# Kernel tuning notes

Measured on AMD Instinct MI355X. Metric: run time of the kernel, lower is better.

## Reference

```python
import jax, jax.numpy as jnp
import numpy as np

W_IMG = 512
H_IMG = 512
D_MODEL = 192
N_FREQ = 8
LN_EPS = 1e-5


def _fourier_pe(coords_norm):
    # coords_norm: [B,K,2] in [0,1); returns [B,K,4*N_FREQ]
    freqs = 2.0 ** jnp.arange(N_FREQ, dtype=jnp.float32)  # [F]
    two_pi = 2.0 * jnp.pi
    x = coords_norm[..., 0:1] * freqs * two_pi  # [B,K,F]
    y = coords_norm[..., 1:2] * freqs * two_pi
    return jnp.concatenate([jnp.sin(x), jnp.cos(x), jnp.sin(y), jnp.cos(y)], axis=-1)


def _bilinear_sample(feat, gx, gy):
    # feat: [B,C,H,W]; gx,gy: [B,K] normalized coords in [-1,1], align_corners=True
    B, C, H, W = feat.shape
    ix = (gx + 1.0) * 0.5 * (W - 1)
    iy = (gy + 1.0) * 0.5 * (H - 1)
    ix0 = jnp.floor(ix)
    iy0 = jnp.floor(iy)
    wx = ix - ix0  # [B,K]
    wy = iy - iy0
    x0 = jnp.clip(ix0.astype(jnp.int32), 0, W - 1)
    x1 = jnp.clip(ix0.astype(jnp.int32) + 1, 0, W - 1)
    y0 = jnp.clip(iy0.astype(jnp.int32), 0, H - 1)
    y1 = jnp.clip(iy0.astype(jnp.int32) + 1, 0, H - 1)
    b = jnp.arange(B)[:, None]  # [B,1] broadcast against [B,K]
    g = lambda y, x: feat[b, :, y, x]  # [B,K,C]
    out = (g(y0, x0) * ((1 - wx) * (1 - wy))[..., None]
           + g(y0, x1) * (wx * (1 - wy))[..., None]
           + g(y1, x0) * ((1 - wx) * wy)[..., None]
           + g(y1, x1) * (wx * wy)[..., None])
    return out  # [B,K,C]


def setup_inputs() -> dict:
    key = jax.random.key(0)
    ks = jax.random.split(key, 16)
    B, K = 8, 4096
    # pixel coordinates in [0, W_IMG-1] x [0, H_IMG-1]
    u = jax.random.uniform(ks[0], (B, K, 2), dtype=jnp.float32)
    coords = u * jnp.array([W_IMG - 1, H_IMG - 1], dtype=jnp.float32)
    L1 = jax.random.normal(ks[1], (B, D_MODEL, 128, 128), dtype=jnp.float32)
    L2 = jax.random.normal(ks[2], (B, D_MODEL, 64, 64), dtype=jnp.float32)
    L3 = jax.random.normal(ks[3], (B, D_MODEL, 32, 32), dtype=jnp.float32)
    L4 = jax.random.normal(ks[4], (B, D_MODEL, 16, 16), dtype=jnp.float32)
    d_in = D_MODEL * 4 + 4 * N_FREQ  # 800
    Wseed_w = jax.random.normal(ks[5], (D_MODEL, d_in), dtype=jnp.float32) / np.sqrt(d_in)
    Wseed_b = jnp.zeros((D_MODEL,), dtype=jnp.float32)
    ln_g = jnp.ones((D_MODEL,), dtype=jnp.float32)
    ln_b = jnp.zeros((D_MODEL,), dtype=jnp.float32)
    Wpos_w = jax.random.normal(ks[6], (D_MODEL, 4 * N_FREQ), dtype=jnp.float32) / np.sqrt(4 * N_FREQ)
    Wpos_b = jnp.zeros((D_MODEL,), dtype=jnp.float32)
    return {"coords": coords, "L1": L1, "L2": L2, "L3": L3, "L4": L4,
            "Wseed_w": Wseed_w, "Wseed_b": Wseed_b, "ln_g": ln_g, "ln_b": ln_b,
            "Wpos_w": Wpos_w, "Wpos_b": Wpos_b}


def reference(coords, L1, L2, L3, L4, Wseed_w, Wseed_b, ln_g, ln_b, Wpos_w, Wpos_b):
    B, K, _ = coords.shape
    # normalized grid in [-1,1] (x uses W, y uses H), align_corners=True convention
    gx = 2.0 * coords[..., 0] / (W_IMG - 1) - 1.0  # [B,K]
    gy = 2.0 * coords[..., 1] / (H_IMG - 1) - 1.0
    center_grid = jnp.stack([gx, gy], axis=-1).reshape(B, K, 1, 2)
    coords_norm = coords / jnp.array([W_IMG, H_IMG], dtype=jnp.float32)
    pe_q = _fourier_pe(coords_norm)  # [B,K,32]
    f1 = _bilinear_sample(L1, gx, gy)
    f2 = _bilinear_sample(L2, gx, gy)
    f3 = _bilinear_sample(L3, gx, gy)
    f4 = _bilinear_sample(L4, gx, gy)
    x = jnp.concatenate([f1, f2, f3, f4, pe_q], axis=-1)  # [B,K,800]
    seed = x @ Wseed_w.T + Wseed_b
    mu = jnp.mean(seed, axis=-1, keepdims=True)
    var = jnp.mean((seed - mu) ** 2, axis=-1, keepdims=True)
    seed = (seed - mu) / jnp.sqrt(var + LN_EPS) * ln_g + ln_b
    pos = pe_q @ Wpos_w.T + Wpos_b
    return (seed, pos, center_grid)
```

## Files before the change

kernel.cpp:

```cpp
#include <hip/hip_runtime.h>
#include <hip/hip_bf16.h>
#include <stdint.h>

typedef unsigned short u16;
typedef short s16x8 __attribute__((ext_vector_type(8)));
typedef float f32x4 __attribute__((ext_vector_type(4)));
typedef uint32_t u32x4 __attribute__((ext_vector_type(4)));

__device__ __forceinline__ uint32_t pack_bf16(float lo, float hi) {
  float2 f; f.x = lo; f.y = hi;
  __hip_bfloat162 h = __float22bfloat162_rn(f);
  union { __hip_bfloat162 h; uint32_t u; } c; c.h = h;
  return c.u;
}
__device__ __forceinline__ u16 f2bf(float f) {
  union { float f; uint32_t u; } a; a.f = f;
  uint32_t u = a.u;
  return (u16)((u + 0x7fffu + ((u >> 16) & 1u)) >> 16);
}
__device__ __forceinline__ float bf2f(uint32_t hbits) {
  union { uint32_t u; float f; } a; a.u = hbits << 16;
  return a.f;
}

__global__ __launch_bounds__(256) void prep_all(
    const float* __restrict__ L1, const float* __restrict__ L2,
    const float* __restrict__ L3, const float* __restrict__ L4,
    const float* __restrict__ ws_w, const float* __restrict__ wp_w,
    u16* __restrict__ T1, u16* __restrict__ T2,
    u16* __restrict__ T3, u16* __restrict__ T4,
    u16* __restrict__ dWs, u16* __restrict__ dWp) {
  const int bid = blockIdx.x;
  const int t = threadIdx.x;

  if (bid >= 2720) {
    int t0 = (bid - 2720) * 256 + t;
    for (int i = t0; i < 39936; i += 8192) {
      const float* s; u16* d; int off;
      if (i < 38400) { s = ws_w; d = dWs; off = 4 * i; }
      else           { s = wp_w; d = dWp; off = 4 * (i - 38400); }
      f32x4 v = *(const f32x4*)(s + off);
      uint2 o;
      o.x = pack_bf16(v.x, v.y);
      o.y = pack_bf16(v.z, v.w);
      *(uint2*)(d + off) = o;
    }
    return;
  }

  const float* src; u16* dst; int HW, tiles, rel;
  if (bid < 2048)      { src = L1; dst = T1; HW = 16384; tiles = 256; rel = bid; }
  else if (bid < 2560) { src = L2; dst = T2; HW = 4096;  tiles = 64;  rel = bid - 2048; }
  else if (bid < 2688) { src = L3; dst = T3; HW = 1024;  tiles = 16;  rel = bid - 2560; }
  else                 { src = L4; dst = T4; HW = 256;   tiles = 4;   rel = bid - 2688; }
  const int b = rel / tiles, hw0 = (rel % tiles) * 64;

  __shared__ uint32_t tileD[96 * 65];
  const float* sb = src + (size_t)b * 192 * HW + hw0;
  for (int i = 0; i < 6; ++i) {
    int idx = i * 256 + t;
    int c2 = idx >> 4, hw4 = idx & 15;
    f32x4 a = *(const f32x4*)(sb + (size_t)(2 * c2) * HW + hw4 * 4);
    f32x4 c = *(const f32x4*)(sb + (size_t)(2 * c2 + 1) * HW + hw4 * 4);
    uint32_t* w = &tileD[c2 * 65 + hw4 * 4];
    w[0] = pack_bf16(a.x, c.x);
    w[1] = pack_bf16(a.y, c.y);
    w[2] = pack_bf16(a.z, c.z);
    w[3] = pack_bf16(a.w, c.w);
  }
  __syncthreads();
  uint32_t* d = (uint32_t*)(dst + ((size_t)b * HW + hw0) * 192);
  for (int i = 0; i < 12; ++i) {
    int e = i * 256 + t;
    int hw = e / 48, cp = e - hw * 48;
    uint2 v;
    v.x = tileD[(cp * 2) * 65 + hw];
    v.y = tileD[(cp * 2 + 1) * 65 + hw];
    *(uint2*)(d + hw * 96 + cp * 2) = v;
  }
}

__global__ __launch_bounds__(256, 4) void seed_main(
    const float* __restrict__ coords,
    const u16* __restrict__ T1, const u16* __restrict__ T2,
    const u16* __restrict__ T3, const u16* __restrict__ T4,
    const u16* __restrict__ Wseed, const u16* __restrict__ Wpos,
    const float* __restrict__ seed_b, const float* __restrict__ ln_g,
    const float* __restrict__ ln_b, const float* __restrict__ pos_b,
    float* __restrict__ out_seed, float* __restrict__ out_pos,
    float* __restrict__ out_cg) {

  __shared__ __align__(16) u16 xt[16 * 808];
  __shared__ float mu_s[16], rs_s[16];

  const int t = threadIdx.x;
  const int gp0 = blockIdx.x * 16;
  const int b = gp0 >> 12;

  if (t < 32) {
    int p = t >> 1, xy = t & 1;
    float c = coords[(gp0 + p) * 2 + xy];
    out_cg[(gp0 + p) * 2 + xy] = c * (2.0f / 511.0f) - 1.0f;
  }
  for (int i = 0; i < 2; ++i) {
    int e = i * 256 + t;
    int p = e >> 5, j = e & 31;
    float c = coords[(gp0 + p) * 2 + ((j >> 4) & 1)] * (1.0f / 512.0f);
    float v = c * (float)(1 << (j & 7));
    float a = (v - floorf(v)) * 6.283185307179586f;
    float r = (j & 8) ? __cosf(a) : __sinf(a);
    xt[p * 808 + 768 + j] = f2bf(r);
  }

  {
    const u16* B1 = T1 + (size_t)b * 16384 * 192;
    const u16* B2 = T2 + (size_t)b * 4096 * 192;
    const u16* B3 = T3 + (size_t)b * 1024 * 192;
    const u16* B4 = T4 + (size_t)b * 256 * 192;
    int plv = t >> 2;
    int lv = plv & 3, p = plv >> 2;
    int c4b = t & 3;
    float cx = coords[(gp0 + p) * 2 + 0];
    float cy = coords[(gp0 + p) * 2 + 1];
    float gx = cx * (2.0f / 511.0f) - 1.0f;
    float gy = cy * (2.0f / 511.0f) - 1.0f;
    int Wl = 128 >> lv;
    float ix = (gx + 1.0f) * 0.5f * (float)(Wl - 1);
    float iy = (gy + 1.0f) * 0.5f * (float)(Wl - 1);
    float fx = floorf(ix), fy = floorf(iy);
    float wx = ix - fx, wy = iy - fy;
    int x0 = (int)fx, y0 = (int)fy;
    int x1 = min(max(x0 + 1, 0), Wl - 1), y1 = min(max(y0 + 1, 0), Wl - 1);
    x0 = min(max(x0, 0), Wl - 1); y0 = min(max(y0, 0), Wl - 1);
    const u16* base = (lv == 0) ? B1 : (lv == 1) ? B2 : (lv == 2) ? B3 : B4;
    const u16* b00 = base + (y0 * Wl + x0) * 192;
    const u16* b01 = base + (y0 * Wl + x1) * 192;
    const u16* b10 = base + (y1 * Wl + x0) * 192;
    const u16* b11 = base + (y1 * Wl + x1) * 192;
    float w00 = (1.0f - wx) * (1.0f - wy), w01 = wx * (1.0f - wy);
    float w10 = (1.0f - wx) * wy,          w11 = wx * wy;
    u16* dstp = xt + p * 808 + lv * 192;
#pragma unroll
    for (int i = 0; i < 6; ++i) {
      int cc = (c4b + 4 * i) * 8;
      u32x4 q00 = *(const u32x4*)(b00 + cc);
      u32x4 q01 = *(const u32x4*)(b01 + cc);
      u32x4 q10 = *(const u32x4*)(b10 + cc);
      u32x4 q11 = *(const u32x4*)(b11 + cc);
      u32x4 o;
#pragma unroll
      for (int k = 0; k < 4; ++k) {
        float lo = bf2f(q00[k] & 0xffff) * w00 + bf2f(q01[k] & 0xffff) * w01 +
                   bf2f(q10[k] & 0xffff) * w10 + bf2f(q11[k] & 0xffff) * w11;
        float hi = bf2f(q00[k] >> 16) * w00 + bf2f(q01[k] >> 16) * w01 +
                   bf2f(q10[k] >> 16) * w10 + bf2f(q11[k] >> 16) * w11;
        o[k] = pack_bf16(lo, hi);
      }
      *(u32x4*)(dstp + cc) = o;
    }
  }
  __syncthreads();

  const int lid = t & 63, wv = t >> 6;
  const int quad = lid >> 4, mrow = lid & 15;
  const int nt0 = wv * 3;

  f32x4 accS[3], accP[3];
#pragma unroll
  for (int j = 0; j < 3; ++j) { accS[j] = (f32x4)0.0f; accP[j] = (f32x4)0.0f; }

  const u16* wp0 = Wseed + (size_t)((nt0 + 0) * 16 + mrow) * 800 + quad * 8;
  const u16* wp1 = wp0 + 16 * 800;
  const u16* wp2 = wp1 + 16 * 800;
  const u16* arow = xt + mrow * 808 + quad * 8;

  s16x8 a_last;
#pragma unroll 5
  for (int kc = 0; kc < 25; ++kc) {
    int ko = kc * 32;
    s16x8 a = *(const s16x8*)(arow + ko);
    s16x8 b0 = *(const s16x8*)(wp0 + ko);
    s16x8 b1 = *(const s16x8*)(wp1 + ko);
    s16x8 b2 = *(const s16x8*)(wp2 + ko);
    accS[0] = __builtin_amdgcn_mfma_f32_16x16x32_bf16(a, b0, accS[0], 0, 0, 0);
    accS[1] = __builtin_amdgcn_mfma_f32_16x16x32_bf16(a, b1, accS[1], 0, 0, 0);
    accS[2] = __builtin_amdgcn_mfma_f32_16x16x32_bf16(a, b2, accS[2], 0, 0, 0);
    if (kc == 24) a_last = a;
  }
#pragma unroll
  for (int j = 0; j < 3; ++j) {
    int n = (nt0 + j) * 16 + mrow;
    s16x8 bw = *(const s16x8*)(Wpos + n * 32 + quad * 8);
    accP[j] = __builtin_amdgcn_mfma_f32_16x16x32_bf16(a_last, bw, accP[j], 0, 0, 0);
  }

#pragma unroll
  for (int j = 0; j < 3; ++j) {
    int n = (nt0 + j) * 16 + mrow;
    float pb = pos_b[n];
#pragma unroll
    for (int r = 0; r < 4; ++r)
      out_pos[(size_t)(gp0 + quad * 4 + r) * 192 + n] = accP[j][r] + pb;
  }

  __syncthreads();
  float* preLN = (float*)xt;
#pragma unroll
  for (int j = 0; j < 3; ++j) {
    int n = (nt0 + j) * 16 + mrow;
    float sb = seed_b[n];
#pragma unroll
    for (int r = 0; r < 4; ++r)
      preLN[(quad * 4 + r) * 193 + n] = accS[j][r] + sb;
  }
  __syncthreads();

  {
    int r = t >> 4, g = t & 15;
    float s = 0.0f, sq = 0.0f;
#pragma unroll
    for (int i = 0; i < 12; ++i) {
      float v = preLN[r * 193 + g * 12 + i];
      s += v; sq += v * v;
    }
#pragma unroll
    for (int d = 8; d > 0; d >>= 1) {
      s += __shfl_down(s, d, 16);
      sq += __shfl_down(sq, d, 16);
    }
    if (g == 0) {
      float mu = s * (1.0f / 192.0f);
      float var = sq * (1.0f / 192.0f) - mu * mu;
      mu_s[r] = mu;
      rs_s[r] = 1.0f / sqrtf(var + 1e-5f);
    }
  }
  __syncthreads();

  for (int i = 0; i < 12; ++i) {
    int e = i * 256 + t;
    int r = e / 192, n = e - r * 192;
    float v = (preLN[r * 193 + n] - mu_s[r]) * rs_s[r] * ln_g[n] + ln_b[n];
    out_seed[(size_t)(gp0 + r) * 192 + n] = v;
  }
}

extern "C" void kernel_launch(void* const* d_in, const int* in_sizes, int n_in,
                              void* d_out, int out_size, void* d_ws, size_t ws_size,
                              hipStream_t stream) {
  const float* coords  = (const float*)d_in[0];
  const float* L1      = (const float*)d_in[1];
  const float* L2      = (const float*)d_in[2];
  const float* L3      = (const float*)d_in[3];
  const float* L4      = (const float*)d_in[4];
  const float* Wseed_w = (const float*)d_in[5];
  const float* Wseed_b = (const float*)d_in[6];
  const float* ln_g    = (const float*)d_in[7];
  const float* ln_b    = (const float*)d_in[8];
  const float* Wpos_w  = (const float*)d_in[9];
  const float* Wpos_b  = (const float*)d_in[10];

  u16* T1  = (u16*)d_ws;
  u16* T2  = T1 + (size_t)8 * 16384 * 192;
  u16* T3  = T2 + (size_t)8 * 4096 * 192;
  u16* T4  = T3 + (size_t)8 * 1024 * 192;
  u16* Wsd = T4 + (size_t)8 * 256 * 192;
  u16* Wps = Wsd + 153600;

  prep_all<<<2752, 256, 0, stream>>>(L1, L2, L3, L4, Wseed_w, Wpos_w,
                                     T1, T2, T3, T4, Wsd, Wps);

  float* out_seed = (float*)d_out;
  float* out_pos  = out_seed + (size_t)32768 * 192;
  float* out_cg   = out_pos  + (size_t)32768 * 192;

  seed_main<<<2048, 256, 0, stream>>>(coords, T1, T2, T3, T4, Wsd, Wps,
                                      Wseed_b, ln_g, ln_b, Wpos_b,
                                      out_seed, out_pos, out_cg);
}
```

Baseline: 274.9 us.

## Pre-swizzle weights into MFMA fragment order and software-pipeline gather and GEMM loads

```diff
diff --git a/kernel.cpp b/kernel.cpp
--- a/kernel.cpp
+++ b/kernel.cpp
@@ -21,6 +21,20 @@
 __device__ __forceinline__ float bf2f(uint32_t hbits) {
   union { uint32_t u; float f; } a; a.u = hbits << 16;
   return a.f;
+}
+
+__device__ __forceinline__ u32x4 bilin4(u32x4 q00, u32x4 q01, u32x4 q10, u32x4 q11,
+                                        float w00, float w01, float w10, float w11) {
+  u32x4 o;
+#pragma unroll
+  for (int k = 0; k < 4; ++k) {
+    float lo = bf2f(q00[k] & 0xffff) * w00 + bf2f(q01[k] & 0xffff) * w01 +
+               bf2f(q10[k] & 0xffff) * w10 + bf2f(q11[k] & 0xffff) * w11;
+    float hi = bf2f(q00[k] >> 16) * w00 + bf2f(q01[k] >> 16) * w01 +
+               bf2f(q10[k] >> 16) * w10 + bf2f(q11[k] >> 16) * w11;
+    o[k] = pack_bf16(lo, hi);
+  }
+  return o;
 }
 
 __global__ __launch_bounds__(256) void prep_all(
@@ -36,14 +50,31 @@
   if (bid >= 2720) {
     int t0 = (bid - 2720) * 256 + t;
     for (int i = t0; i < 39936; i += 8192) {
-      const float* s; u16* d; int off;
-      if (i < 38400) { s = ws_w; d = dWs; off = 4 * i; }
-      else           { s = wp_w; d = dWp; off = 4 * (i - 38400); }
-      f32x4 v = *(const f32x4*)(s + off);
-      uint2 o;
-      o.x = pack_bf16(v.x, v.y);
-      o.y = pack_bf16(v.z, v.w);
-      *(uint2*)(d + off) = o;
+      if (i < 38400) {
+        int e4 = 4 * i;
+        int n = e4 / 800;
+        int k = e4 - n * 800;
+        f32x4 v = *(const f32x4*)(ws_w + e4);
+        int nt = n >> 4, mrow = n & 15;
+        int kc = k >> 5, quad = (k >> 3) & 3, e0 = k & 7;
+        int dst = ((nt * 25 + kc) * 64 + (quad * 16 + mrow)) * 8 + e0;
+        uint2 o;
+        o.x = pack_bf16(v.x, v.y);
+        o.y = pack_bf16(v.z, v.w);
+        *(uint2*)(dWs + dst) = o;
+      } else {
+        int j = i - 38400;
+        int e4 = 4 * j;
+        int n = e4 >> 5, k = e4 & 31;
+        f32x4 v = *(const f32x4*)(wp_w + e4);
+        int nt = n >> 4, mrow = n & 15;
+        int quad = k >> 3, e0 = k & 7;
+        int dst = (nt * 64 + (quad * 16 + mrow)) * 8 + e0;
+        uint2 o;
+        o.x = pack_bf16(v.x, v.y);
+        o.y = pack_bf16(v.z, v.w);
+        *(uint2*)(dWp + dst) = o;
+      }
     }
     return;
   }
@@ -80,7 +111,7 @@
   }
 }
 
-__global__ __launch_bounds__(256, 4) void seed_main(
+__global__ __launch_bounds__(256, 6) void seed_main(
     const float* __restrict__ coords,
     const u16* __restrict__ T1, const u16* __restrict__ T2,
     const u16* __restrict__ T3, const u16* __restrict__ T4,
@@ -140,24 +171,24 @@
     float w00 = (1.0f - wx) * (1.0f - wy), w01 = wx * (1.0f - wy);
     float w10 = (1.0f - wx) * wy,          w11 = wx * wy;
     u16* dstp = xt + p * 808 + lv * 192;
-#pragma unroll
-    for (int i = 0; i < 6; ++i) {
-      int cc = (c4b + 4 * i) * 8;
-      u32x4 q00 = *(const u32x4*)(b00 + cc);
-      u32x4 q01 = *(const u32x4*)(b01 + cc);
-      u32x4 q10 = *(const u32x4*)(b10 + cc);
-      u32x4 q11 = *(const u32x4*)(b11 + cc);
-      u32x4 o;
-#pragma unroll
-      for (int k = 0; k < 4; ++k) {
-        float lo = bf2f(q00[k] & 0xffff) * w00 + bf2f(q01[k] & 0xffff) * w01 +
-                   bf2f(q10[k] & 0xffff) * w10 + bf2f(q11[k] & 0xffff) * w11;
-        float hi = bf2f(q00[k] >> 16) * w00 + bf2f(q01[k] >> 16) * w01 +
-                   bf2f(q10[k] >> 16) * w10 + bf2f(q11[k] >> 16) * w11;
-        o[k] = pack_bf16(lo, hi);
-      }
-      *(u32x4*)(dstp + cc) = o;
-    }
+    int cph = (c4b + lv) & 3;
+    int cc = cph * 8;
+    u32x4 q00 = *(const u32x4*)(b00 + cc);
+    u32x4 q01 = *(const u32x4*)(b01 + cc);
+    u32x4 q10 = *(const u32x4*)(b10 + cc);
+    u32x4 q11 = *(const u32x4*)(b11 + cc);
+#pragma unroll
+    for (int i = 0; i < 5; ++i) {
+      int cn = cc + 32;
+      u32x4 n00 = *(const u32x4*)(b00 + cn);
+      u32x4 n01 = *(const u32x4*)(b01 + cn);
+      u32x4 n10 = *(const u32x4*)(b10 + cn);
+      u32x4 n11 = *(const u32x4*)(b11 + cn);
+      *(u32x4*)(dstp + cc) = bilin4(q00, q01, q10, q11, w00, w01, w10, w11);
+      cc = cn;
+      q00 = n00; q01 = n01; q10 = n10; q11 = n11;
+    }
+    *(u32x4*)(dstp + cc) = bilin4(q00, q01, q10, q11, w00, w01, w10, w11);
   }
   __syncthreads();
 
@@ -165,42 +196,43 @@
   const int quad = lid >> 4, mrow = lid & 15;
   const int nt0 = wv * 3;
 
-  f32x4 accS[3], accP[3];
-#pragma unroll
-  for (int j = 0; j < 3; ++j) { accS[j] = (f32x4)0.0f; accP[j] = (f32x4)0.0f; }
-
-  const u16* wp0 = Wseed + (size_t)((nt0 + 0) * 16 + mrow) * 800 + quad * 8;
-  const u16* wp1 = wp0 + 16 * 800;
-  const u16* wp2 = wp1 + 16 * 800;
+  f32x4 accS[3];
+#pragma unroll
+  for (int j = 0; j < 3; ++j) accS[j] = (f32x4)0.0f;
+
+  const u16* ws = Wseed + (size_t)nt0 * 12800 + lid * 8;
   const u16* arow = xt + mrow * 808 + quad * 8;
 
-  s16x8 a_last;
-#pragma unroll 5
-  for (int kc = 0; kc < 25; ++kc) {
-    int ko = kc * 32;
-    s16x8 a = *(const s16x8*)(arow + ko);
-    s16x8 b0 = *(const s16x8*)(wp0 + ko);
-    s16x8 b1 = *(const s16x8*)(wp1 + ko);
-    s16x8 b2 = *(const s16x8*)(wp2 + ko);
+  s16x8 a  = *(const s16x8*)(arow);
+  s16x8 b0 = *(const s16x8*)(ws);
+  s16x8 b1 = *(const s16x8*)(ws + 12800);
+  s16x8 b2 = *(const s16x8*)(ws + 25600);
+#pragma unroll 6
+  for (int kc = 0; kc < 24; ++kc) {
+    s16x8 an = *(const s16x8*)(arow + (kc + 1) * 32);
+    const u16* wp = ws + (kc + 1) * 512;
+    s16x8 b0n = *(const s16x8*)(wp);
+    s16x8 b1n = *(const s16x8*)(wp + 12800);
+    s16x8 b2n = *(const s16x8*)(wp + 25600);
     accS[0] = __builtin_amdgcn_mfma_f32_16x16x32_bf16(a, b0, accS[0], 0, 0, 0);
     accS[1] = __builtin_amdgcn_mfma_f32_16x16x32_bf16(a, b1, accS[1], 0, 0, 0);
     accS[2] = __builtin_amdgcn_mfma_f32_16x16x32_bf16(a, b2, accS[2], 0, 0, 0);
-    if (kc == 24) a_last = a;
-  }
+    a = an; b0 = b0n; b1 = b1n; b2 = b2n;
+  }
+  accS[0] = __builtin_amdgcn_mfma_f32_16x16x32_bf16(a, b0, accS[0], 0, 0, 0);
+  accS[1] = __builtin_amdgcn_mfma_f32_16x16x32_bf16(a, b1, accS[1], 0, 0, 0);
+  accS[2] = __builtin_amdgcn_mfma_f32_16x16x32_bf16(a, b2, accS[2], 0, 0, 0);
+
 #pragma unroll
   for (int j = 0; j < 3; ++j) {
-    int n = (nt0 + j) * 16 + mrow;
-    s16x8 bw = *(const s16x8*)(Wpos + n * 32 + quad * 8);
-    accP[j] = __builtin_amdgcn_mfma_f32_16x16x32_bf16(a_last, bw, accP[j], 0, 0, 0);
-  }
-
-#pragma unroll
-  for (int j = 0; j < 3; ++j) {
+    s16x8 bw = *(const s16x8*)(Wpos + (size_t)(nt0 + j) * 512 + lid * 8);
+    f32x4 ap = (f32x4)0.0f;
+    ap = __builtin_amdgcn_mfma_f32_16x16x32_bf16(a, bw, ap, 0, 0, 0);
     int n = (nt0 + j) * 16 + mrow;
     float pb = pos_b[n];
 #pragma unroll
     for (int r = 0; r < 4; ++r)
-      out_pos[(size_t)(gp0 + quad * 4 + r) * 192 + n] = accP[j][r] + pb;
+      out_pos[(size_t)(gp0 + quad * 4 + r) * 192 + n] = ap[r] + pb;
   }
 
   __syncthreads();
```

After: 255.3 us. -7.1%, faster.
